# Kernel optimization log

Hardware: AMD Instinct MI355X
Metric: run time of the kernel (lower is better)

The kernel has to match this reference:

```python
import jax, jax.numpy as jnp
import numpy as np

T, N, IN, H, OUT, B = 250, 256, 1024, 1024, 35, 4
IN_B = IN // B
V_TH = 1.0  # spikingjelly LIFNode defaults: v_threshold=1.0, v_reset=0.0, decay_input=True


def heaviside(x):
    return (x >= 0.0).astype(x.dtype)


def setup_inputs() -> dict:
    key = jax.random.key(0)
    ks = jax.random.split(key, 9)
    x = jax.random.normal(ks[0], (T, N, IN), dtype=jnp.float32)
    # branch Linear(IN_B, H) stacked over branches: weight [B, IN_B, H], bias [B, H]
    Wb = jax.random.normal(ks[1], (B, IN_B, H), dtype=jnp.float32) / np.sqrt(IN_B)
    bb = jax.random.normal(ks[2], (B, H), dtype=jnp.float32) * 0.01
    # branch_taus ~ U(2, 6), shape [B, H]
    taus = jax.random.uniform(ks[3], (B, H), dtype=jnp.float32, minval=2.0, maxval=6.0)
    W2 = jax.random.normal(ks[4], (H, OUT), dtype=jnp.float32) / np.sqrt(H)
    b2 = jax.random.normal(ks[5], (OUT,), dtype=jnp.float32) * 0.01
    # learnable membrane time constants ~ U(0.5, 4) (clipped away from 0 for stability)
    tau1 = jax.random.uniform(ks[6], (1,), dtype=jnp.float32, minval=0.5, maxval=4.0)
    tau2 = jax.random.uniform(ks[7], (1,), dtype=jnp.float32, minval=0.5, maxval=4.0)
    return {"x": x, "Wb": Wb, "bb": bb, "taus": taus, "W2": W2, "b2": b2,
            "tau1": tau1, "tau2": tau2}


def reference(x, Wb, bb, taus, W2, b2, tau1, tau2):
    alpha = jax.nn.sigmoid(taus)  # [B, H] dendritic leak gates

    def step(carry, x_t):
        state, v1, v2, acc = carry
        # split input into contiguous branch chunks: [N, B, IN_B]
        xr = x_t.reshape(N, B, IN_B)
        branch_in = jnp.einsum('nbi,bih->nbh', xr, Wb) + bb  # [N, B, H]
        state = alpha * state + (1.0 - alpha) * branch_in     # leaky dendritic integration
        combined = state.sum(axis=1)                          # [N, H]
        # LIF1: charge (decay_input), fire (heaviside), hard reset (detach_reset)
        v1 = v1 + (combined - v1) / tau1
        s1 = heaviside(v1 - V_TH)
        v1 = v1 * (1.0 - s1)
        h2 = s1 @ W2 + b2                                     # [N, OUT]
        v2 = v2 + (h2 - v2) / tau2
        s2 = heaviside(v2 - V_TH)
        v2 = v2 * (1.0 - s2)
        return (state, v1, v2, acc + s2), None

    init = (jnp.zeros((N, B, H), x.dtype), jnp.zeros((N, H), x.dtype),
            jnp.zeros((N, OUT), x.dtype), jnp.zeros((N, OUT), x.dtype))
    (_, _, _, out_sum), _ = jax.lax.scan(step, init, x)
    return jax.nn.log_softmax(out_sum, axis=1)
```

## Files before the change

kernel.cpp:

```cpp
#include <hip/hip_runtime.h>
#include <cstdint>
#include <cstddef>


typedef __bf16 bf16;
typedef __bf16 bf16x8 __attribute__((ext_vector_type(8)));
typedef float  f32x4  __attribute__((ext_vector_type(4)));

#define Tt    250
#define Nn    256
#define Hh    1024
#define OUTK  35
#define NBR   4

#define OFF_FLAG 0u
#define OFF_WBT  256u
#define OFF_W2T  2097408u
#define OFF_ALF  2195712u
#define OFF_OMF  2212096u
#define OFF_BBF  2228480u
#define OFF_B2S  2244864u
#define OFF_H2   2245120u
#define OFF_STW  14533120u
#define OFF_V1W  18727424u
#define OFF_S1P  19776000u
#define OFF_BIN  27968000u
#define FIXED_WS 27968000u

__device__ __forceinline__ float ld_in(const void* p, size_t i, int f32) {
    return f32 ? ((const float*)p)[i] : (float)((const bf16*)p)[i];
}

__device__ __forceinline__ void gload16(const void* g, void* l) {
    __builtin_amdgcn_global_load_lds(
        (const __attribute__((address_space(1))) void*)g,
        (__attribute__((address_space(3))) void*)l, 16, 0, 0);
}

__global__ void sniff_kernel(const unsigned short* __restrict__ x,
                             int* __restrict__ flag) {
    int cnt = 0;
    for (int i = threadIdx.x; i < 4096; i += 64) {
        int e = (x[i] >> 7) & 0xFF;
        cnt += (e >= 100 && e <= 140) ? 1 : 0;
    }
#pragma unroll
    for (int o = 32; o > 0; o >>= 1) cnt += __shfl_xor(cnt, o);
    if (threadIdx.x == 0) *flag = (cnt < 3400) ? 1 : 0;
}

__global__ void trans_wb_kernel(const void* __restrict__ Wb, bf16* __restrict__ WbT,
                                const int* __restrict__ flagp) {
    int f32 = *flagp;
    __shared__ bf16 tile[32][33];
    int bid = blockIdx.x;
    int b   = bid >> 8;
    int rem = bid & 255;
    int kt  = rem >> 5;
    int htl = rem & 31;
    int tx = threadIdx.x & 31, ty = threadIdx.x >> 5;
#pragma unroll
    for (int i = 0; i < 4; ++i) {
        int k = kt * 32 + ty + i * 8;
        int h = htl * 32 + tx;
        tile[ty + i * 8][tx] = (bf16)ld_in(Wb, (size_t)(b * 256 + k) * 1024 + h, f32);
    }
    __syncthreads();
#pragma unroll
    for (int i = 0; i < 4; ++i) {
        int h = htl * 32 + ty + i * 8;
        int k = kt * 32 + tx;
        WbT[((size_t)b * 1024 + h) * 256 + k] = tile[tx][ty + i * 8];
    }
}

__global__ void trans_w2_kernel(const void* __restrict__ W2, bf16* __restrict__ W2T,
                                const int* __restrict__ flagp) {
    int f32 = *flagp;
    int idx = blockIdx.x * 256 + threadIdx.x;
    int c = idx >> 10;
    int k = idx & 1023;
    W2T[idx] = (c < OUTK) ? (bf16)ld_in(W2, (size_t)k * OUTK + c, f32) : (bf16)0.0f;
}

__global__ void prep_kernel(const void* taus, const void* bb, const void* b2,
                            const void* tau1, const void* tau2,
                            float* alf, float* omf, float* bbf, float* b2s,
                            const int* __restrict__ flagp) {
    int f32 = *flagp;
    int idx = blockIdx.x * 256 + threadIdx.x;
    if (idx < 4096) {
        float tv = ld_in(taus, idx, f32);
        float a = 1.0f / (1.0f + expf(-tv));
        alf[idx] = a;
        omf[idx] = 1.0f - a;
        bbf[idx] = ld_in(bb, idx, f32);
    } else if (idx < 4144) {
        int c = idx - 4096;
        b2s[c] = (c < OUTK) ? ld_in(b2, c, f32) : 0.0f;
    } else if (idx == 4144) {
        b2s[48] = ld_in(tau1, 0, f32);
    } else if (idx == 4145) {
        b2s[49] = ld_in(tau2, 0, f32);
    }
}

__global__ __launch_bounds__(256, 2)
void gemm1_kernel(const void* __restrict__ xsrc,
                  const bf16* __restrict__ BT, bf16* __restrict__ C,
                  const int* __restrict__ flagp, int TCl) {
    __shared__ bf16 Alds[2][4096];
    __shared__ bf16 Blds[2][4096];
    int f32 = *flagp;
    int tid = threadIdx.x;
    int tiles_pb = TCl * 16;

    int nwg = gridDim.x;
    int bid = blockIdx.x;
    int tile = ((nwg & 7) == 0) ? ((bid & 7) * (nwg >> 3) + (bid >> 3)) : bid;

    int branch = tile / tiles_pb;
    int rem = tile % tiles_pb;
    int mt = rem >> 3, ht = rem & 7;
    int w = tid >> 6, lane = tid & 63;
    int l15 = lane & 15, l4 = lane >> 4;
    int wm = w >> 1, wh = w & 1;
    const int m0 = mt * 128, h0 = ht * 128;

    const int row = tid >> 2;
    const int q   = tid & 3;
    const int swr = (tid >> 3) & 3;
    const int srd = (l15 >> 1) & 3;

    f32x4 zero = {0.f, 0.f, 0.f, 0.f};
    f32x4 acc[4][4];
#pragma unroll
    for (int mi = 0; mi < 4; ++mi)
#pragma unroll
        for (int hi = 0; hi < 4; ++hi) acc[mi][hi] = zero;

    const bf16* Bbase = BT + (size_t)branch * (1024 * 256) + (size_t)h0 * 256;

    float4 anxt[2][2];
    bf16x8 bnxt[2];

    auto issueB = [&](int kc, int pp) {
#pragma unroll
        for (int r = 0; r < 2; ++r)
            gload16(Bbase + (size_t)(r * 64 + row) * 256 + kc * 32 + (q ^ swr) * 8,
                    &Blds[pp][(size_t)(r * 256 + tid) * 8]);
    };
    auto issueA = [&](int kc) {
        if (f32) {
#pragma unroll
            for (int r = 0; r < 2; ++r) {
                const float4* pa = (const float4*)((const float*)xsrc +
                    ((size_t)(m0 + r * 64 + row) * 1024 + branch * 256 + kc * 32 + q * 8));
                anxt[r][0] = pa[0];
                anxt[r][1] = pa[1];
            }
        } else {
#pragma unroll
            for (int r = 0; r < 2; ++r)
                bnxt[r] = *(const bf16x8*)((const bf16*)xsrc +
                    ((size_t)(m0 + r * 64 + row) * 1024 + branch * 256 + kc * 32 + q * 8));
        }
    };
    auto writeA = [&](int pp) {
#pragma unroll
        for (int r = 0; r < 2; ++r) {
            bf16x8 av;
            if (f32) {
                float4 u0 = anxt[r][0], u1 = anxt[r][1];
                av[0] = (bf16)u0.x; av[1] = (bf16)u0.y;
                av[2] = (bf16)u0.z; av[3] = (bf16)u0.w;
                av[4] = (bf16)u1.x; av[5] = (bf16)u1.y;
                av[6] = (bf16)u1.z; av[7] = (bf16)u1.w;
            } else {
                av = bnxt[r];
            }
            *(bf16x8*)&Alds[pp][(size_t)(r * 64 + row) * 32 + (q ^ swr) * 8] = av;
        }
    };

    issueB(0, 0);
    issueA(0);
    asm volatile("s_waitcnt vmcnt(0)" ::: "memory");
    writeA(0);
    asm volatile("s_waitcnt lgkmcnt(0)" ::: "memory");
    __builtin_amdgcn_s_barrier();

#pragma unroll
    for (int kc = 0; kc < 8; ++kc) {
        const int p = kc & 1;
        if (kc < 7) {
            issueB(kc + 1, p ^ 1);
            issueA(kc + 1);
        }
        __builtin_amdgcn_sched_barrier(0);
        bf16x8 af[4], bfr[4];
#pragma unroll
        for (int mi = 0; mi < 4; ++mi)
            af[mi] = *(const bf16x8*)&Alds[p][(wm * 64 + mi * 16 + l15) * 32 + (l4 ^ srd) * 8];
#pragma unroll
        for (int hi = 0; hi < 4; ++hi)
            bfr[hi] = *(const bf16x8*)&Blds[p][(wh * 64 + hi * 16 + l15) * 32 + (l4 ^ srd) * 8];
#pragma unroll
        for (int mi = 0; mi < 4; ++mi)
#pragma unroll
            for (int hi = 0; hi < 4; ++hi)
                acc[mi][hi] = __builtin_amdgcn_mfma_f32_16x16x32_bf16(
                    af[mi], bfr[hi], acc[mi][hi], 0, 0, 0);
        if (kc < 7) {
            asm volatile("s_waitcnt vmcnt(0)" ::: "memory");
            writeA(p ^ 1);
            asm volatile("s_waitcnt lgkmcnt(0)" ::: "memory");
        } else {
            asm volatile("s_waitcnt lgkmcnt(0)" ::: "memory");
        }
        __builtin_amdgcn_s_barrier();
    }

    bf16* Cb = C + (size_t)branch * ((size_t)TCl * 256 * 1024);
#pragma unroll
    for (int mi = 0; mi < 4; ++mi)
#pragma unroll
        for (int hi = 0; hi < 4; ++hi) {
            int rr = m0 + wm * 64 + mi * 16 + l4 * 4;
            int col = h0 + wh * 64 + hi * 16 + l15;
#pragma unroll
            for (int r = 0; r < 4; ++r)
                Cb[(size_t)(rr + r) * 1024 + col] = (bf16)acc[mi][hi][r];
        }
}

template<int TCC>
__global__ void scan_kernel(const bf16* __restrict__ bin,
                            const float* __restrict__ alf,
                            const float* __restrict__ omf,
                            const float* __restrict__ bbf,
                            const float* __restrict__ b2s,
                            unsigned long long* __restrict__ s1p,
                            float* __restrict__ stw,
                            float* __restrict__ v1w,
                            int t0, int TCl_rt) {
    const int TCl = TCC ? TCC : TCl_rt;
    int n = blockIdx.x >> 2;
    int h = (blockIdx.x & 3) * 256 + threadIdx.x;
    int lane = threadIdx.x & 63;
    int widx = (blockIdx.x & 3) * 4 + (threadIdx.x >> 6);
    size_t CHEc = (size_t)TCl * 256 * 1024;
    size_t base = (size_t)n * 1024 + h;

    float al[NBR], om[NBR], bbv[NBR], st[NBR];
    float v1;
#pragma unroll
    for (int b = 0; b < NBR; ++b) {
        al[b] = alf[b * Hh + h];
        om[b] = omf[b * Hh + h];
        bbv[b] = bbf[b * Hh + h];
    }
    if (t0 == 0) {
#pragma unroll
        for (int b = 0; b < NBR; ++b) st[b] = 0.f;
        v1 = 0.f;
    } else {
#pragma unroll
        for (int b = 0; b < NBR; ++b)
            st[b] = stw[((size_t)b * Nn + n) * Hh + h];
        v1 = v1w[(size_t)n * Hh + h];
    }
    float tau1 = b2s[48];

    float nxt[NBR];
#pragma unroll
    for (int b = 0; b < NBR; ++b) nxt[b] = (float)bin[b * CHEc + base];

#pragma unroll 2
    for (int tl = 0; tl < TCl; ++tl) {
        float cur[NBR];
#pragma unroll
        for (int b = 0; b < NBR; ++b) cur[b] = nxt[b];
        if (tl + 1 < TCl) {
            size_t nb = base + (size_t)(tl + 1) * (256 * 1024);
#pragma unroll
            for (int b = 0; b < NBR; ++b) nxt[b] = (float)bin[b * CHEc + nb];
        }
#pragma unroll
        for (int b = 0; b < NBR; ++b)
            st[b] = al[b] * st[b] + om[b] * (cur[b] + bbv[b]);
        float comb = st[0] + st[1] + st[2] + st[3];
        v1 += (comb - v1) / tau1;
        bool sp = (v1 >= 1.0f);
        unsigned long long m = __ballot(sp);
        if (lane == 0)
            s1p[((size_t)(t0 + tl) * Nn + n) * 16 + widx] = m;
        if (sp) v1 = 0.f;
    }
#pragma unroll
    for (int b = 0; b < NBR; ++b) stw[((size_t)b * Nn + n) * Hh + h] = st[b];
    v1w[(size_t)n * Hh + h] = v1;
}

__global__ __launch_bounds__(256, 2)
void gemm2_kernel(const unsigned char* __restrict__ s1b,
                  const bf16* __restrict__ W2T, float* __restrict__ h2) {
    __shared__ bf16 Alds[4096];
    __shared__ bf16 Blds[1536];
    int tid = threadIdx.x;
    int m0 = blockIdx.x * 128;
    int w = tid >> 6, lane = tid & 63;
    int l15 = lane & 15, l4 = lane >> 4;

    f32x4 zero = {0.f, 0.f, 0.f, 0.f};
    f32x4 acc[2][3];
#pragma unroll
    for (int mi = 0; mi < 2; ++mi)
#pragma unroll
        for (int hi = 0; hi < 3; ++hi) acc[mi][hi] = zero;

    const bf16 ONE = (bf16)1.0f, ZER = (bf16)0.0f;

    for (int kc = 0; kc < 32; ++kc) {
        bf16x8 av[2], bv;
#pragma unroll
        for (int r = 0; r < 2; ++r) {
            int L = r * 256 + tid;
            int row = L >> 2;
            unsigned char bits = s1b[(size_t)(m0 + row) * 128 + kc * 4 + (L & 3)];
#pragma unroll
            for (int j = 0; j < 8; ++j)
                av[r][j] = ((bits >> j) & 1) ? ONE : ZER;
        }
        if (tid < 192)
            bv = *(const bf16x8*)&W2T[(size_t)(tid >> 2) * 1024 + kc * 32 + (tid & 3) * 8];
        __syncthreads();
#pragma unroll
        for (int r = 0; r < 2; ++r)
            *(bf16x8*)&Alds[(size_t)(r * 256 + tid) * 8] = av[r];
        if (tid < 192)
            *(bf16x8*)&Blds[(size_t)tid * 8] = bv;
        __syncthreads();
        bf16x8 af[2], bfr[3];
#pragma unroll
        for (int mi = 0; mi < 2; ++mi)
            af[mi] = *(const bf16x8*)&Alds[(w * 32 + mi * 16 + l15) * 32 + l4 * 8];
#pragma unroll
        for (int hi = 0; hi < 3; ++hi)
            bfr[hi] = *(const bf16x8*)&Blds[(hi * 16 + l15) * 32 + l4 * 8];
#pragma unroll
        for (int mi = 0; mi < 2; ++mi)
#pragma unroll
            for (int hi = 0; hi < 3; ++hi)
                acc[mi][hi] = __builtin_amdgcn_mfma_f32_16x16x32_bf16(
                    af[mi], bfr[hi], acc[mi][hi], 0, 0, 0);
        __syncthreads();
    }
#pragma unroll
    for (int mi = 0; mi < 2; ++mi)
#pragma unroll
        for (int hi = 0; hi < 3; ++hi) {
            int col = hi * 16 + l15;
#pragma unroll
            for (int r = 0; r < 4; ++r) {
                int m = m0 + w * 32 + mi * 16 + l4 * 4 + r;
                int t = m >> 8;
                int n = m & 255;
                h2[((size_t)n * Tt + t) * 48 + col] = acc[mi][hi][r];
            }
        }
}

__global__ void out_kernel(const float* __restrict__ h2,
                           const float* __restrict__ b2s,
                           float* __restrict__ out) {
    int n = blockIdx.x;
    int k = threadIdx.x;
    float b2v = (k < 48) ? b2s[k] : 0.f;
    float tau2 = b2s[49];
    float v2 = 0.f, acc = 0.f;
    const float* base = h2 + (size_t)n * Tt * 48;
    for (int t = 0; t < Tt; ++t) {
        float hv = (k < 48) ? base[t * 48 + k] : 0.f;
        hv += b2v;
        v2 += (hv - v2) / tau2;
        bool sp = (v2 >= 1.0f);
        if (sp) { acc += 1.f; v2 = 0.f; }
    }
    float val = (k < OUTK) ? acc : -3.0e38f;
    float mx = val;
#pragma unroll
    for (int o = 32; o > 0; o >>= 1) mx = fmaxf(mx, __shfl_xor(mx, o));
    float e = (k < OUTK) ? expf(val - mx) : 0.f;
    float s = e;
#pragma unroll
    for (int o = 32; o > 0; o >>= 1) s += __shfl_xor(s, o);
    if (k < OUTK) out[n * OUTK + k] = (val - mx) - logf(s);
}

extern "C" void kernel_launch(void* const* d_in, const int* in_sizes, int n_in,
                              void* d_out, int out_size, void* d_ws, size_t ws_size,
                              hipStream_t stream) {
    const void* x    = d_in[0];
    const void* Wb   = d_in[1];
    const void* bb   = d_in[2];
    const void* taus = d_in[3];
    const void* W2   = d_in[4];
    const void* b2   = d_in[5];
    const void* tau1 = d_in[6];
    const void* tau2 = d_in[7];
    float* out = (float*)d_out;

    char* ws = (char*)d_ws;
    int*   flag = (int*)(ws + OFF_FLAG);
    bf16*  WbT  = (bf16*)(ws + OFF_WBT);
    bf16*  W2T  = (bf16*)(ws + OFF_W2T);
    float* alf  = (float*)(ws + OFF_ALF);
    float* omf  = (float*)(ws + OFF_OMF);
    float* bbf  = (float*)(ws + OFF_BBF);
    float* b2s  = (float*)(ws + OFF_B2S);
    float* h2   = (float*)(ws + OFF_H2);
    float* stw  = (float*)(ws + OFF_STW);
    float* v1w  = (float*)(ws + OFF_V1W);
    unsigned long long* s1p = (unsigned long long*)(ws + OFF_S1P);
    bf16*  bin  = (bf16*)(ws + OFF_BIN);

    const int cands[8] = {250, 125, 50, 25, 10, 5, 2, 1};
    int TC = 1;
    for (int i = 0; i < 8; ++i) {
        size_t need = (size_t)FIXED_WS + (size_t)cands[i] * 2097152u;
        if (need <= ws_size) { TC = cands[i]; break; }
    }

    sniff_kernel<<<1, 64, 0, stream>>>((const unsigned short*)x, flag);
    trans_wb_kernel<<<1024, 256, 0, stream>>>(Wb, WbT, flag);
    trans_w2_kernel<<<192, 256, 0, stream>>>(W2, W2T, flag);
    prep_kernel<<<17, 256, 0, stream>>>(taus, bb, b2, tau1, tau2,
                                        alf, omf, bbf, b2s, flag);

    int nch = Tt / TC;
    for (int c = 0; c < nch; ++c) {
        const void* xc = (const void*)((const char*)x +
            (size_t)c * TC * 256 * 1024 * 4);
        gemm1_kernel<<<64 * TC, 256, 0, stream>>>(xc, WbT, bin, flag, TC);
        if (TC == 250)
            scan_kernel<250><<<1024, 256, 0, stream>>>(
                bin, alf, omf, bbf, b2s, s1p, stw, v1w, c * TC, TC);
        else
            scan_kernel<0><<<1024, 256, 0, stream>>>(
                bin, alf, omf, bbf, b2s, s1p, stw, v1w, c * TC, TC);
    }
    gemm2_kernel<<<500, 256, 0, stream>>>((const unsigned char*)s1p, W2T, h2);
    out_kernel<<<Nn, 64, 0, stream>>>(h2, b2s, out);

    (void)in_sizes; (void)n_in; (void)out_size;
}
```

Before: 899.1 us.

## Deepen gemm1 global-load pipeline to triple-buffered LDS with prefetch distance two

Turns the gemm1 K-loop from double buffering into triple-buffered LDS stages. Loads for chunk k+2 are issued while chunk k computes, and partial vmcnt waits stop the loop from draining all outstanding loads every iteration. This is meant to hide more global-memory latency. It costs more LDS (48KB per block), which may reduce occupancy at two blocks per CU, plus extra registers for the second A staging slot.

```diff
diff --git a/kernel.cpp b/kernel.cpp
--- a/kernel.cpp
+++ b/kernel.cpp
@@ -109,8 +109,8 @@
 void gemm1_kernel(const void* __restrict__ xsrc,
                   const bf16* __restrict__ BT, bf16* __restrict__ C,
                   const int* __restrict__ flagp, int TCl) {
-    __shared__ bf16 Alds[2][4096];
-    __shared__ bf16 Blds[2][4096];
+    __shared__ bf16 Alds[3][4096];
+    __shared__ bf16 Blds[3][4096];
     int f32 = *flagp;
     int tid = threadIdx.x;
     int tiles_pb = TCl * 16;
@@ -141,8 +141,8 @@
 
     const bf16* Bbase = BT + (size_t)branch * (1024 * 256) + (size_t)h0 * 256;
 
-    float4 anxt[2][2];
-    bf16x8 bnxt[2];
+    float4 anxt[2][2][2];
+    bf16x8 bnxt[2][2];
 
     auto issueB = [&](int kc, int pp) {
 #pragma unroll
@@ -150,52 +150,51 @@
             gload16(Bbase + (size_t)(r * 64 + row) * 256 + kc * 32 + (q ^ swr) * 8,
                     &Blds[pp][(size_t)(r * 256 + tid) * 8]);
     };
-    auto issueA = [&](int kc) {
+    auto issueA = [&](int kc, int sl) {
         if (f32) {
 #pragma unroll
             for (int r = 0; r < 2; ++r) {
                 const float4* pa = (const float4*)((const float*)xsrc +
                     ((size_t)(m0 + r * 64 + row) * 1024 + branch * 256 + kc * 32 + q * 8));
-                anxt[r][0] = pa[0];
-                anxt[r][1] = pa[1];
+                anxt[sl][r][0] = pa[0];
+                anxt[sl][r][1] = pa[1];
             }
         } else {
 #pragma unroll
             for (int r = 0; r < 2; ++r)
-                bnxt[r] = *(const bf16x8*)((const bf16*)xsrc +
+                bnxt[sl][r] = *(const bf16x8*)((const bf16*)xsrc +
                     ((size_t)(m0 + r * 64 + row) * 1024 + branch * 256 + kc * 32 + q * 8));
         }
     };
-    auto writeA = [&](int pp) {
+    auto writeA = [&](int pp, int sl) {
 #pragma unroll
         for (int r = 0; r < 2; ++r) {
             bf16x8 av;
             if (f32) {
-                float4 u0 = anxt[r][0], u1 = anxt[r][1];
+                float4 u0 = anxt[sl][r][0], u1 = anxt[sl][r][1];
                 av[0] = (bf16)u0.x; av[1] = (bf16)u0.y;
                 av[2] = (bf16)u0.z; av[3] = (bf16)u0.w;
                 av[4] = (bf16)u1.x; av[5] = (bf16)u1.y;
                 av[6] = (bf16)u1.z; av[7] = (bf16)u1.w;
             } else {
-                av = bnxt[r];
+                av = bnxt[sl][r];
             }
             *(bf16x8*)&Alds[pp][(size_t)(r * 64 + row) * 32 + (q ^ swr) * 8] = av;
         }
     };
 
-    issueB(0, 0);
-    issueA(0);
-    asm volatile("s_waitcnt vmcnt(0)" ::: "memory");
-    writeA(0);
-    asm volatile("s_waitcnt lgkmcnt(0)" ::: "memory");
-    __builtin_amdgcn_s_barrier();
+    issueB(0, 0); issueA(0, 0);
+    issueB(1, 1); issueA(1, 1);
+    asm volatile("s_waitcnt vmcnt(4)" ::: "memory");
+    writeA(0, 0);
+    asm volatile("s_waitcnt lgkmcnt(0)\ns_barrier" ::: "memory");
 
 #pragma unroll
     for (int kc = 0; kc < 8; ++kc) {
-        const int p = kc & 1;
-        if (kc < 7) {
-            issueB(kc + 1, p ^ 1);
-            issueA(kc + 1);
+        const int p = kc % 3;
+        if (kc + 2 < 8) {
+            issueB(kc + 2, (kc + 2) % 3);
+            issueA(kc + 2, (kc + 2) & 1);
         }
         __builtin_amdgcn_sched_barrier(0);
         bf16x8 af[4], bfr[4];
@@ -212,13 +211,13 @@
                 acc[mi][hi] = __builtin_amdgcn_mfma_f32_16x16x32_bf16(
                     af[mi], bfr[hi], acc[mi][hi], 0, 0, 0);
         if (kc < 7) {
-            asm volatile("s_waitcnt vmcnt(0)" ::: "memory");
-            writeA(p ^ 1);
-            asm volatile("s_waitcnt lgkmcnt(0)" ::: "memory");
-        } else {
-            asm volatile("s_waitcnt lgkmcnt(0)" ::: "memory");
-        }
-        __builtin_amdgcn_s_barrier();
+            if (kc + 2 < 8)
+                asm volatile("s_waitcnt vmcnt(4)" ::: "memory");
+            else
+                asm volatile("s_waitcnt vmcnt(0)" ::: "memory");
+            writeA((kc + 1) % 3, (kc + 1) & 1);
+            asm volatile("s_waitcnt lgkmcnt(0)\ns_barrier" ::: "memory");
+        }
     }
 
     bf16* Cb = C + (size_t)branch * ((size_t)TCl * 256 * 1024);
```

Measured after the change: 894.9 us. About the same (-0.5%).
